# Performance work log

Hardware: AMD Instinct MI355X
Metric: run time of the kernel (lower is better)

Reference implementation:

```python
import jax, jax.numpy as jnp
import numpy as np

B, L, H, N, COND = 32, 32768, 32, 16, 4
N2 = N // 2  # S4D stores N/2 complex conjugate-pair modes


def setup_inputs() -> dict:
    key = jax.random.key(0)
    ks = jax.random.split(key, 8)
    x = jax.random.normal(ks[0], (B, L, H), jnp.float32)
    cond = jax.random.normal(ks[1], (B, COND), jnp.float32)
    # S4D kernel parameters (state-spaces minimal S4D init)
    log_dt = np.log(1e-3) + jax.random.uniform(ks[2], (H,), jnp.float32) * (np.log(1e-1) - np.log(1e-3))
    C_re = jax.random.normal(ks[3], (H, N2), jnp.float32) * (0.5 ** 0.5)
    C_im = jax.random.normal(ks[4], (H, N2), jnp.float32) * (0.5 ** 0.5)
    log_A_real = jnp.log(0.5 * jnp.ones((H, N2), jnp.float32))
    A_imag = jnp.pi * jnp.tile(jnp.arange(N2, dtype=jnp.float32), (H, 1))
    D = jax.random.normal(ks[5], (H,), jnp.float32)
    # FiLM linear: cond -> (gamma, beta)
    film_W = jax.random.normal(ks[6], (COND, 2 * H), jnp.float32) / np.sqrt(COND)
    film_b = jnp.zeros((2 * H,), jnp.float32)
    return dict(x=x, cond=cond, log_dt=log_dt, C_re=C_re, C_im=C_im,
                log_A_real=log_A_real, A_imag=A_imag, D=D,
                film_W=film_W, film_b=film_b)


def reference(x, cond, log_dt, C_re, C_im, log_A_real, A_imag, D, film_W, film_b):
    # x: (B, L, H) -> DSSM over channel-major layout (B, H, L)
    u = jnp.transpose(x, (0, 2, 1))  # B H L
    # --- S4D kernel: K[h, l] = 2 * Re( sum_n C~_hn * exp(dt_h * A_hn * l) )
    dt = jnp.exp(log_dt)[:, None]                      # (H, 1)
    A = -jnp.exp(log_A_real) + 1j * A_imag             # (H, N2) complex
    dtA = A * dt                                       # (H, N2)
    Ct = (C_re + 1j * C_im) * (jnp.exp(dtA) - 1.0) / A # discretized C
    vand = jnp.exp(dtA[:, :, None] * jnp.arange(L, dtype=jnp.float32))  # (H, N2, L)
    K = 2.0 * jnp.einsum('hn,hnl->hl', Ct, vand).real  # (H, L)
    # --- causal convolution via FFT on length-2L circular pad
    n_fft = 2 * L
    y = jnp.fft.irfft(jnp.fft.rfft(u, n=n_fft) * jnp.fft.rfft(K, n=n_fft), n=n_fft)[..., :L]
    y = y + u * D[:, None]                             # skip connection
    y = jnp.transpose(y, (0, 2, 1))                    # back to (B, L, H)
    # --- FiLM conditioning
    gb = cond @ film_W + film_b                        # (B, 2H)
    gamma, beta = gb[:, :H], gb[:, H:]
    y = gamma[:, None, :] * y + beta[:, None, :]
    # --- activation
    return jax.nn.gelu(y)
```

## Files before the change

kernel.cpp:

```cpp
#include <hip/hip_runtime.h>

typedef float v2f __attribute__((ext_vector_type(2)));

#define BB 32
#define LL 32768
#define HH 32
#define NN2 8
#define NCOND 4
#define NCHUNK 256
#define LC (LL / NCHUNK)

#define PARAM_OFF 0
#define WLC_OFF   1024
#define FILM_OFF  1536
#define S_OFF     4096
#define SZ_S      (BB * HH * NCHUNK * 16)

static __device__ __forceinline__ v2f vfma(v2f a, v2f b, v2f c) {
  return __builtin_elementwise_fma(a, b, c);
}

__global__ void setup_kernel(const float* __restrict__ log_dt,
                             const float* __restrict__ C_re,
                             const float* __restrict__ C_im,
                             const float* __restrict__ log_A_real,
                             const float* __restrict__ A_imag,
                             const float* __restrict__ cond,
                             const float* __restrict__ film_W,
                             const float* __restrict__ film_b,
                             float* __restrict__ ws) {
  int idx = blockIdx.x * blockDim.x + threadIdx.x;
  if (idx < HH * NN2) {
    int h = idx >> 3, n = idx & (NN2 - 1);
    float dt = expf(log_dt[h]);
    float ar = -expf(log_A_real[idx]);
    float ai = A_imag[idx];
    float dr = ar * dt, di = ai * dt;
    float er = expf(dr);
    float wr = er * cosf(di);
    float wi = er * sinf(di);
    float den = ar * ar + ai * ai;
    float tr = ((wr - 1.f) * ar + wi * ai) / den;
    float ti = (wi * ar - (wr - 1.f) * ai) / den;
    float cr = C_re[idx], ci = C_im[idx];
    float ctr = 2.f * (cr * tr - ci * ti);
    float cti = 2.f * (cr * ti + ci * tr);
    float* p = ws + PARAM_OFF + h * 32;
    p[n] = wr; p[n + 8] = wi; p[n + 16] = ctr; p[n + 24] = cti;
    float eL  = expf(dr * (float)LC);
    float wlr = eL * cosf(di * (float)LC);
    float wli = eL * sinf(di * (float)LC);
    float* q = ws + WLC_OFF + idx * 2;
    q[0] = wlr; q[1] = wli;
  }
  int f = idx - HH * NN2;
  if (f >= 0 && f < BB * HH) {
    int b = f >> 5, h = f & (HH - 1);
    float g  = film_b[h];
    float be = film_b[h + HH];
    #pragma unroll
    for (int c2 = 0; c2 < NCOND; c2++) {
      float cv = cond[b * NCOND + c2];
      g  = fmaf(cv, film_W[c2 * 2 * HH + h], g);
      be = fmaf(cv, film_W[c2 * 2 * HH + HH + h], be);
    }
    float* p = ws + FILM_OFF + f * 2;
    p[0] = g; p[1] = be;
  }
}

__global__ __launch_bounds__(256) void pass_a(const float* __restrict__ x,
                                              float* __restrict__ ws) {
  const int flat = blockIdx.x * 256 + threadIdx.x;
  const int h = flat & (HH - 1);
  const int c = (flat >> 5) & (NCHUNK - 1);
  const int b = flat >> 13;
  const v2f* pp = (const v2f*)(ws + PARAM_OFF + h * 32);
  v2f wr[4], wi[4], zr[4], zi[4];
  #pragma unroll
  for (int g = 0; g < 4; g++) {
    wr[g] = pp[g]; wi[g] = pp[4 + g];
    zr[g] = (v2f){0.f, 0.f}; zi[g] = (v2f){0.f, 0.f};
  }
  const float* xp = x + ((size_t)b * LL + (size_t)c * LC) * HH + h;
  for (int i = 0; i < LC; i += 8) {
    float u[8];
    #pragma unroll
    for (int j = 0; j < 8; j++) u[j] = xp[(size_t)(i + j) * HH];
    #pragma unroll
    for (int j = 0; j < 8; j++) {
      v2f us = (v2f){u[j], u[j]};
      #pragma unroll
      for (int g = 0; g < 4; g++) {
        v2f t0  = vfma(-wi[g], zi[g], us);
        v2f nzr = vfma(wr[g], zr[g], t0);
        v2f nzi = vfma(wr[g], zi[g], wi[g] * zr[g]);
        zr[g] = nzr; zi[g] = nzi;
      }
    }
  }
  v2f* Sp = (v2f*)(ws + S_OFF + (size_t)flat * 16);
  #pragma unroll
  for (int g = 0; g < 4; g++) { Sp[g] = zr[g]; Sp[4 + g] = zi[g]; }
}

__global__ void pass_b(float* __restrict__ ws) {
  int idx = blockIdx.x * blockDim.x + threadIdx.x;
  int n = idx & (NN2 - 1);
  int h = (idx >> 3) & (HH - 1);
  int b = idx >> 8;
  float wlr = ws[WLC_OFF + (h * NN2 + n) * 2];
  float wli = ws[WLC_OFF + (h * NN2 + n) * 2 + 1];
  float Zr = 0.f, Zi = 0.f;
  const size_t stride = (size_t)HH * 16;
  size_t base = ((size_t)b * NCHUNK * HH + h) * 16 + n;
  for (int c = 0; c < NCHUNK; c++) {
    float* pr = ws + S_OFF + base + (size_t)c * stride;
    float sr = pr[0];
    float si = pr[8];
    pr[0] = Zr;
    pr[8] = Zi;
    float nZr = fmaf(wlr, Zr, fmaf(-wli, Zi, sr));
    float nZi = fmaf(wlr, Zi, fmaf(wli, Zr, si));
    Zr = nZr; Zi = nZi;
  }
}

__global__ __launch_bounds__(256) void pass_c(const float* __restrict__ x,
                                              const float* __restrict__ Dv,
                                              float* __restrict__ out,
                                              float* __restrict__ ws) {
  const int flat = blockIdx.x * 256 + threadIdx.x;
  const int h = flat & (HH - 1);
  const int c = (flat >> 5) & (NCHUNK - 1);
  const int b = flat >> 13;
  const v2f* pp = (const v2f*)(ws + PARAM_OFF + h * 32);
  v2f wr[4], wi[4], ctr[4], cti[4], zr[4], zi[4];
  #pragma unroll
  for (int g = 0; g < 4; g++) {
    wr[g] = pp[g]; wi[g] = pp[4 + g]; ctr[g] = pp[8 + g]; cti[g] = pp[12 + g];
  }
  const v2f* Zp = (const v2f*)(ws + S_OFF + (size_t)flat * 16);
  #pragma unroll
  for (int g = 0; g < 4; g++) { zr[g] = Zp[g]; zi[g] = Zp[4 + g]; }
  float gamma = ws[FILM_OFF + ((size_t)b * HH + h) * 2];
  float beta  = ws[FILM_OFF + ((size_t)b * HH + h) * 2 + 1];
  float dcoef = Dv[h];
  const size_t off = ((size_t)b * LL + (size_t)c * LC) * HH + h;
  const float* xp = x + off;
  float* op = out + off;
  for (int i = 0; i < LC; i += 8) {
    float u[8];
    #pragma unroll
    for (int j = 0; j < 8; j++) u[j] = xp[(size_t)(i + j) * HH];
    #pragma unroll
    for (int j = 0; j < 8; j++) {
      v2f us = (v2f){u[j], u[j]};
      v2f acc = (v2f){0.f, 0.f};
      #pragma unroll
      for (int g = 0; g < 4; g++) {
        v2f t0  = vfma(-wi[g], zi[g], us);
        v2f nzr = vfma(wr[g], zr[g], t0);
        v2f nzi = vfma(wr[g], zi[g], wi[g] * zr[g]);
        zr[g] = nzr; zi[g] = nzi;
        acc = vfma(ctr[g], nzr, acc);
        acc = vfma(-cti[g], nzi, acc);
      }
      float y = acc.x + acc.y;
      y = fmaf(dcoef, u[j], y);
      y = fmaf(gamma, y, beta);
      float y3   = y * y * y;
      float targ = 0.7978845608f * fmaf(0.044715f, y3, y);
      float e    = __expf(2.f * targ);
      float th   = 1.f - __fdividef(2.f, e + 1.f);
      op[(size_t)(i + j) * HH] = 0.5f * y * (1.f + th);
    }
  }
}

extern "C" void kernel_launch(void* const* d_in, const int* in_sizes, int n_in,
                              void* d_out, int out_size, void* d_ws, size_t ws_size,
                              hipStream_t stream) {
  const float* x          = (const float*)d_in[0];
  const float* cond       = (const float*)d_in[1];
  const float* log_dt     = (const float*)d_in[2];
  const float* C_re       = (const float*)d_in[3];
  const float* C_im       = (const float*)d_in[4];
  const float* log_A_real = (const float*)d_in[5];
  const float* A_imag     = (const float*)d_in[6];
  const float* Dv         = (const float*)d_in[7];
  const float* film_W     = (const float*)d_in[8];
  const float* film_b     = (const float*)d_in[9];
  float* out = (float*)d_out;
  float* ws  = (float*)d_ws;

  setup_kernel<<<5, 256, 0, stream>>>(log_dt, C_re, C_im, log_A_real, A_imag,
                                      cond, film_W, film_b, ws);
  pass_a<<<(BB * HH * NCHUNK) / 256, 256, 0, stream>>>(x, ws);
  pass_b<<<(BB * HH * NN2) / 256, 256, 0, stream>>>(ws);
  pass_c<<<(BB * HH * NCHUNK) / 256, 256, 0, stream>>>(x, Dv, out, ws);
}
```

Before: 313.8 us.

## Parallelize chunk-state scan with wavefront prefix scan and double chunk count

```diff
diff --git a/kernel.cpp b/kernel.cpp
--- a/kernel.cpp
+++ b/kernel.cpp
@@ -7,7 +7,7 @@
 #define HH 32
 #define NN2 8
 #define NCOND 4
-#define NCHUNK 256
+#define NCHUNK 512
 #define LC (LL / NCHUNK)
 
 #define PARAM_OFF 0
@@ -74,7 +74,7 @@
   const int flat = blockIdx.x * 256 + threadIdx.x;
   const int h = flat & (HH - 1);
   const int c = (flat >> 5) & (NCHUNK - 1);
-  const int b = flat >> 13;
+  const int b = flat >> 14;
   const v2f* pp = (const v2f*)(ws + PARAM_OFF + h * 32);
   v2f wr[4], wi[4], zr[4], zi[4];
   #pragma unroll
@@ -104,24 +104,56 @@
   for (int g = 0; g < 4; g++) { Sp[g] = zr[g]; Sp[4 + g] = zi[g]; }
 }
 
-__global__ void pass_b(float* __restrict__ ws) {
-  int idx = blockIdx.x * blockDim.x + threadIdx.x;
-  int n = idx & (NN2 - 1);
-  int h = (idx >> 3) & (HH - 1);
-  int b = idx >> 8;
-  float wlr = ws[WLC_OFF + (h * NN2 + n) * 2];
-  float wli = ws[WLC_OFF + (h * NN2 + n) * 2 + 1];
-  float Zr = 0.f, Zi = 0.f;
-  const size_t stride = (size_t)HH * 16;
-  size_t base = ((size_t)b * NCHUNK * HH + h) * 16 + n;
-  for (int c = 0; c < NCHUNK; c++) {
-    float* pr = ws + S_OFF + base + (size_t)c * stride;
-    float sr = pr[0];
-    float si = pr[8];
-    pr[0] = Zr;
-    pr[8] = Zi;
-    float nZr = fmaf(wlr, Zr, fmaf(-wli, Zi, sr));
-    float nZi = fmaf(wlr, Zi, fmaf(wli, Zr, si));
+__global__ __launch_bounds__(256) void pass_b(float* __restrict__ ws) {
+  const int wid  = (blockIdx.x * 256 + threadIdx.x) >> 6;
+  const int lane = threadIdx.x & 63;
+  const int n = wid & (NN2 - 1);
+  const int h = (wid >> 3) & (HH - 1);
+  const int b = wid >> 8;
+  const float wlr = ws[WLC_OFF + (h * NN2 + n) * 2];
+  const float wli = ws[WLC_OFF + (h * NN2 + n) * 2 + 1];
+  float sr[8], si[8];
+  const size_t base16 = ((size_t)b * NCHUNK + (size_t)lane * 8) * HH + h;
+  float* sp = ws + S_OFF + base16 * 16 + n;
+  #pragma unroll
+  for (int j = 0; j < 8; j++) {
+    sr[j] = sp[(size_t)j * HH * 16];
+    si[j] = sp[(size_t)j * HH * 16 + 8];
+  }
+  float Tr = 0.f, Ti = 0.f;
+  #pragma unroll
+  for (int j = 0; j < 8; j++) {
+    float nTr = fmaf(wlr, Tr, fmaf(-wli, Ti, sr[j]));
+    float nTi = fmaf(wlr, Ti, fmaf(wli, Tr, si[j]));
+    Tr = nTr; Ti = nTi;
+  }
+  float Mr = wlr, Mi = wli;
+  #pragma unroll
+  for (int k = 0; k < 3; k++) {
+    float t = fmaf(Mr, Mr, -(Mi * Mi));
+    Mi = 2.f * Mr * Mi; Mr = t;
+  }
+  #pragma unroll
+  for (int d = 1; d < 64; d <<= 1) {
+    float pr = __shfl_up(Tr, (unsigned)d, 64);
+    float pi = __shfl_up(Ti, (unsigned)d, 64);
+    if (lane >= d) {
+      float nTr = fmaf(Mr, pr, fmaf(-Mi, pi, Tr));
+      float nTi = fmaf(Mr, pi, fmaf(Mi, pr, Ti));
+      Tr = nTr; Ti = nTi;
+    }
+    float t = fmaf(Mr, Mr, -(Mi * Mi));
+    Mi = 2.f * Mr * Mi; Mr = t;
+  }
+  float Zr = __shfl_up(Tr, 1u, 64);
+  float Zi = __shfl_up(Ti, 1u, 64);
+  if (lane == 0) { Zr = 0.f; Zi = 0.f; }
+  #pragma unroll
+  for (int j = 0; j < 8; j++) {
+    sp[(size_t)j * HH * 16]     = Zr;
+    sp[(size_t)j * HH * 16 + 8] = Zi;
+    float nZr = fmaf(wlr, Zr, fmaf(-wli, Zi, sr[j]));
+    float nZi = fmaf(wlr, Zi, fmaf(wli, Zr, si[j]));
     Zr = nZr; Zi = nZi;
   }
 }
@@ -133,7 +165,7 @@
   const int flat = blockIdx.x * 256 + threadIdx.x;
   const int h = flat & (HH - 1);
   const int c = (flat >> 5) & (NCHUNK - 1);
-  const int b = flat >> 13;
+  const int b = flat >> 14;
   const v2f* pp = (const v2f*)(ws + PARAM_OFF + h * 32);
   v2f wr[4], wi[4], ctr[4], cti[4], zr[4], zi[4];
   #pragma unroll
@@ -173,7 +205,7 @@
       float targ = 0.7978845608f * fmaf(0.044715f, y3, y);
       float e    = __expf(2.f * targ);
       float th   = 1.f - __fdividef(2.f, e + 1.f);
-      op[(size_t)(i + j) * HH] = 0.5f * y * (1.f + th);
+      __builtin_nontemporal_store(0.5f * y * (1.f + th), op + (size_t)(i + j) * HH);
     }
   }
 }
@@ -197,6 +229,6 @@
   setup_kernel<<<5, 256, 0, stream>>>(log_dt, C_re, C_im, log_A_real, A_imag,
                                       cond, film_W, film_b, ws);
   pass_a<<<(BB * HH * NCHUNK) / 256, 256, 0, stream>>>(x, ws);
-  pass_b<<<(BB * HH * NN2) / 256, 256, 0, stream>>>(ws);
+  pass_b<<<(BB * HH * NN2 * 64) / 256, 256, 0, stream>>>(ws);
   pass_c<<<(BB * HH * NCHUNK) / 256, 256, 0, stream>>>(x, Dv, out, ws);
 }
```

New measurement: 357.7 us. 1.14x slower.
